# Optimization experiments

Hardware: AMD Instinct MI355X
Metric: run time of the kernel (lower is better)

The kernel has to match this reference:

```python
import jax, jax.numpy as jnp
import numpy as np

D = 512
SCALE = float(np.sqrt(D // 8))  # sqrt(d_k), d_k = d_model/num_heads = 64
EPS = 1e-5


def _ln(x, g, b):
    m = jnp.mean(x, axis=-1, keepdims=True)
    v = jnp.var(x, axis=-1, keepdims=True)
    return (x - m) * jax.lax.rsqrt(v + EPS) * g + b


def setup_inputs() -> dict:
    key = jax.random.key(0)
    ks = jax.random.split(key, 12)
    B, S = 512, 512
    w = lambda k, shp: jax.random.normal(k, shp, dtype=jnp.float32) * 0.02
    return {
        "sentiment_vec": jax.random.normal(ks[0], (B, D), dtype=jnp.float32),
        "price_sequence": jax.random.normal(ks[1], (B, S, D), dtype=jnp.float32),
        "Wq": w(ks[2], (D, D)), "bq": jnp.zeros((D,), jnp.float32),
        "Wk": w(ks[3], (D, D)), "bk": jnp.zeros((D,), jnp.float32),
        "Wv": w(ks[4], (D, D)), "bv": jnp.zeros((D,), jnp.float32),
        "Wo": w(ks[5], (D, D)), "bo": jnp.zeros((D,), jnp.float32),
        "Wg": w(ks[6], (2 * D, D)), "bg": jnp.zeros((D,), jnp.float32),
        "g_q": jnp.ones((D,), jnp.float32), "beta_q": jnp.zeros((D,), jnp.float32),
        "g_kv": jnp.ones((D,), jnp.float32), "beta_kv": jnp.zeros((D,), jnp.float32),
    }


def reference(sentiment_vec, price_sequence, Wq, bq, Wk, bk, Wv, bv, Wo, bo,
              Wg, bg, g_q, beta_q, g_kv, beta_kv):
    # LayerNorms (query is a single token per batch element)
    Q = _ln(sentiment_vec, g_q, beta_q)            # [B, D]
    KV = _ln(price_sequence, g_kv, beta_kv)        # [B, S, D]
    # Projections (note: forward never splits heads -> single-head attention)
    q = Q @ Wq + bq                                # [B, D]
    k = KV @ Wk + bk                               # [B, S, D]
    v = KV @ Wv + bv                               # [B, S, D]
    # Single-query attention
    scores = jnp.einsum('bd,bsd->bs', q, k) / SCALE
    attn = jax.nn.softmax(scores, axis=-1)         # [B, S] (dropout: eval mode)
    ctx = jnp.einsum('bs,bsd->bd', attn, v)        # [B, D]
    ctx = ctx @ Wo + bo
    # Sigmoid gate over concat([sentiment, context])
    gate_in = jnp.concatenate([sentiment_vec, ctx], axis=-1)  # [B, 2D]
    alpha = jax.nn.sigmoid(gate_in @ Wg + bg)
    fused = alpha * ctx + (1.0 - alpha) * sentiment_vec
    return fused, attn
```

## Files before the change

### kernel.cpp

```cpp
#include <hip/hip_runtime.h>

#define NB 512
#define NS 512
#define ND 512
#define INV_SCALE 0.125f
#define LN_EPS 1e-5f

typedef __attribute__((ext_vector_type(8))) short short8;
typedef __attribute__((ext_vector_type(4))) short short4v;
typedef __attribute__((ext_vector_type(4))) float float4v;

static __device__ __forceinline__ unsigned short f2bf(float x) {
    unsigned int u = __float_as_uint(x);
    unsigned int r = (u + 0x7fffu + ((u >> 16) & 1u)) >> 16;
    return (unsigned short)r;
}
static __device__ __forceinline__ float bf2f(unsigned short h) {
    return __uint_as_float(((unsigned int)h) << 16);
}

__global__ __launch_bounds__(64) void ln_rows_k(const float* __restrict__ x,
                                                const float* __restrict__ g,
                                                const float* __restrict__ be,
                                                float* __restrict__ y) {
    const int row = blockIdx.x;
    const int lane = threadIdx.x;
    const float* xr = x + (size_t)row * ND;
    float4 x0 = *(const float4*)(xr + 4 * lane);
    float4 x1 = *(const float4*)(xr + 256 + 4 * lane);
    float s1 = x0.x + x0.y + x0.z + x0.w + x1.x + x1.y + x1.z + x1.w;
    float s2 = x0.x * x0.x + x0.y * x0.y + x0.z * x0.z + x0.w * x0.w +
               x1.x * x1.x + x1.y * x1.y + x1.z * x1.z + x1.w * x1.w;
    for (int off = 32; off; off >>= 1) {
        s1 += __shfl_xor(s1, off, 64);
        s2 += __shfl_xor(s2, off, 64);
    }
    float mean = s1 * (1.f / 512.f);
    float rstd = rsqrtf(s2 * (1.f / 512.f) - mean * mean + LN_EPS);
    float4 g0 = *(const float4*)(g + 4 * lane);
    float4 g1 = *(const float4*)(g + 256 + 4 * lane);
    float4 b0 = *(const float4*)(be + 4 * lane);
    float4 b1 = *(const float4*)(be + 256 + 4 * lane);
    float4 y0, y1;
    y0.x = (x0.x - mean) * rstd * g0.x + b0.x;
    y0.y = (x0.y - mean) * rstd * g0.y + b0.y;
    y0.z = (x0.z - mean) * rstd * g0.z + b0.z;
    y0.w = (x0.w - mean) * rstd * g0.w + b0.w;
    y1.x = (x1.x - mean) * rstd * g1.x + b1.x;
    y1.y = (x1.y - mean) * rstd * g1.y + b1.y;
    y1.z = (x1.z - mean) * rstd * g1.z + b1.z;
    y1.w = (x1.w - mean) * rstd * g1.w + b1.w;
    float* yr = y + (size_t)row * ND;
    *(float4*)(yr + 4 * lane) = y0;
    *(float4*)(yr + 256 + 4 * lane) = y1;
}

__global__ __launch_bounds__(64) void rowdot_k(const float* __restrict__ q,
                                               const float* __restrict__ bk,
                                               float* __restrict__ s0) {
    const int row = blockIdx.x;
    const int lane = threadIdx.x;
    const float* qr = q + (size_t)row * ND;
    float4 a0 = *(const float4*)(qr + 4 * lane);
    float4 a1 = *(const float4*)(qr + 256 + 4 * lane);
    float4 c0 = *(const float4*)(bk + 4 * lane);
    float4 c1 = *(const float4*)(bk + 256 + 4 * lane);
    float d = a0.x * c0.x + a0.y * c0.y + a0.z * c0.z + a0.w * c0.w +
              a1.x * c1.x + a1.y * c1.y + a1.z * c1.z + a1.w * c1.w;
    for (int off = 32; off; off >>= 1) d += __shfl_xor(d, off, 64);
    if (lane == 0) s0[row] = d;
}

template <bool TRANS_B, int EPI>
__global__ __launch_bounds__(256) void gemm32_k(
    const float* __restrict__ A1, const float* __restrict__ A2, int ksplit,
    const float* __restrict__ B, const float* __restrict__ bias,
    float* __restrict__ C, int M, int N, int K,
    const float* __restrict__ e_ctx, const float* __restrict__ e_sent) {
    constexpr int LDK = 40;
    __shared__ __align__(16) unsigned short Ah[32 * LDK];
    __shared__ __align__(16) unsigned short Al[32 * LDK];
    __shared__ __align__(16) unsigned short Bh[32 * LDK];
    __shared__ __align__(16) unsigned short Bl[32 * LDK];
    const int t = threadIdx.x;
    const int wave = t >> 6, lane = t & 63;
    const int m0 = blockIdx.y * 32, n0 = blockIdx.x * 32;
    const int wm = (wave & 1) * 16, wn = (wave >> 1) * 16;

    float4v acc = (float4v){0.f, 0.f, 0.f, 0.f};

    const int arow = wm + (lane & 15);
    const int brow = wn + (lane & 15);
    const int kq8 = (lane >> 4) * 8;

    const int srow = t >> 3, skq = (t & 7) * 4;

    float4 va, vb;
    {
        int kg = skq;
        if (kg < ksplit)
            va = *(const float4*)(A1 + (size_t)(m0 + srow) * ksplit + kg);
        else
            va = *(const float4*)(A2 + (size_t)(m0 + srow) * (K - ksplit) + (kg - ksplit));
        if (TRANS_B)
            vb = *(const float4*)(B + (size_t)(n0 + srow) * K + skq);
        else
            vb = *(const float4*)(B + (size_t)srow * N + n0 + skq);
    }

    for (int k0 = 0; k0 < K; k0 += 32) {
        {
            unsigned short h0 = f2bf(va.x), h1 = f2bf(va.y), h2 = f2bf(va.z), h3 = f2bf(va.w);
            short4v hv = {(short)h0, (short)h1, (short)h2, (short)h3};
            short4v lv = {(short)f2bf(va.x - bf2f(h0)), (short)f2bf(va.y - bf2f(h1)),
                          (short)f2bf(va.z - bf2f(h2)), (short)f2bf(va.w - bf2f(h3))};
            *(short4v*)&Ah[srow * LDK + skq] = hv;
            *(short4v*)&Al[srow * LDK + skq] = lv;
        }
        if (TRANS_B) {
            unsigned short h0 = f2bf(vb.x), h1 = f2bf(vb.y), h2 = f2bf(vb.z), h3 = f2bf(vb.w);
            short4v hv = {(short)h0, (short)h1, (short)h2, (short)h3};
            short4v lv = {(short)f2bf(vb.x - bf2f(h0)), (short)f2bf(vb.y - bf2f(h1)),
                          (short)f2bf(vb.z - bf2f(h2)), (short)f2bf(vb.w - bf2f(h3))};
            *(short4v*)&Bh[srow * LDK + skq] = hv;
            *(short4v*)&Bl[srow * LDK + skq] = lv;
        } else {
            float vv[4] = {vb.x, vb.y, vb.z, vb.w};
#pragma unroll
            for (int j = 0; j < 4; ++j) {
                unsigned short hh = f2bf(vv[j]);
                Bh[(skq + j) * LDK + srow] = hh;
                Bl[(skq + j) * LDK + srow] = f2bf(vv[j] - bf2f(hh));
            }
        }
        float4 va2, vb2;
        if (k0 + 32 < K) {
            int kg = k0 + 32 + skq;
            if (kg < ksplit)
                va2 = *(const float4*)(A1 + (size_t)(m0 + srow) * ksplit + kg);
            else
                va2 = *(const float4*)(A2 + (size_t)(m0 + srow) * (K - ksplit) + (kg - ksplit));
            if (TRANS_B)
                vb2 = *(const float4*)(B + (size_t)(n0 + srow) * K + k0 + 32 + skq);
            else
                vb2 = *(const float4*)(B + (size_t)(k0 + 32 + srow) * N + n0 + skq);
        } else {
            va2 = va; vb2 = vb;
        }
        __syncthreads();
        short8 ah = *(const short8*)&Ah[arow * LDK + kq8];
        short8 al = *(const short8*)&Al[arow * LDK + kq8];
        short8 bh = *(const short8*)&Bh[brow * LDK + kq8];
        short8 bl = *(const short8*)&Bl[brow * LDK + kq8];
        acc = __builtin_amdgcn_mfma_f32_16x16x32_bf16(ah, bh, acc, 0, 0, 0);
        acc = __builtin_amdgcn_mfma_f32_16x16x32_bf16(ah, bl, acc, 0, 0, 0);
        acc = __builtin_amdgcn_mfma_f32_16x16x32_bf16(al, bh, acc, 0, 0, 0);
        __syncthreads();
        va = va2; vb = vb2;
    }

    const int coln = lane & 15, rbase = (lane >> 4) * 4;
    const int n = n0 + wn + coln;
    const float bv = bias ? bias[n] : 0.f;
#pragma unroll
    for (int r = 0; r < 4; ++r) {
        int m = m0 + wm + rbase + r;
        float val = acc[r] + bv;
        if (EPI == 1) {
            float a = 1.f / (1.f + __expf(-val));
            float cx = e_ctx[(size_t)m * N + n];
            float sv = e_sent[(size_t)m * N + n];
            val = a * cx + (1.f - a) * sv;
        }
        C[(size_t)m * N + n] = val;
    }
}

__global__ __launch_bounds__(512) void flash_k(const float* __restrict__ ps,
                                               const float* __restrict__ g,
                                               const float* __restrict__ be,
                                               const float* __restrict__ qp,
                                               const float* __restrict__ s0v,
                                               float* __restrict__ ctx_pre,
                                               float* __restrict__ attn) {
    const int b = blockIdx.x;
    const int t = threadIdx.x;
    const int wave = t >> 6, lane = t & 63;
    __shared__ float zbuf[NS];
    __shared__ float ubuf[8][ND];
    __shared__ float lw[8], tw[8];

    const float* qb = qp + (size_t)b * ND;
    float4 q0 = *(const float4*)(qb + 4 * lane);
    float4 q1 = *(const float4*)(qb + 256 + 4 * lane);
    float4 g0 = *(const float4*)(g + 4 * lane);
    float4 g1 = *(const float4*)(g + 256 + 4 * lane);
    float4 b0 = *(const float4*)(be + 4 * lane);
    float4 b1 = *(const float4*)(be + 256 + 4 * lane);

    float4 qg0, qg1;
    qg0.x = g0.x * q0.x; qg0.y = g0.y * q0.y; qg0.z = g0.z * q0.z; qg0.w = g0.w * q0.w;
    qg1.x = g1.x * q1.x; qg1.y = g1.y * q1.y; qg1.z = g1.z * q1.z; qg1.w = g1.w * q1.w;
    float c1 = qg0.x + qg0.y + qg0.z + qg0.w + qg1.x + qg1.y + qg1.z + qg1.w;
    float c2 = b0.x * q0.x + b0.y * q0.y + b0.z * q0.z + b0.w * q0.w +
               b1.x * q1.x + b1.y * q1.y + b1.z * q1.z + b1.w * q1.w;
    for (int off = 32; off; off >>= 1) {
        c1 += __shfl_xor(c1, off, 64);
        c2 += __shfl_xor(c2, off, 64);
    }
    const float K2 = INV_SCALE * (c2 + s0v[b]);
    const float C1 = c1;

    float l = 0.f, t1 = 0.f;
    float4 u0 = {0.f, 0.f, 0.f, 0.f}, u1 = {0.f, 0.f, 0.f, 0.f};

    const float* base = ps + ((size_t)b * NS + wave * 64) * ND + 4 * lane;
    float4 xa0 = *(const float4*)(base);
    float4 xa1 = *(const float4*)(base + 256);
    float4 xb0 = *(const float4*)(base + ND);
    float4 xb1 = *(const float4*)(base + ND + 256);

    for (int r = 0; r < 64; r += 2) {
        float4 ya0, ya1, yb0, yb1;
        if (r < 62) {
            const float* nb = base + (size_t)(r + 2) * ND;
            ya0 = *(const float4*)(nb);
            ya1 = *(const float4*)(nb + 256);
            yb0 = *(const float4*)(nb + ND);
            yb1 = *(const float4*)(nb + ND + 256);
        } else {
            ya0 = xa0; ya1 = xa1; yb0 = xb0; yb1 = xb1;
        }
        float sa1 = xa0.x + xa0.y + xa0.z + xa0.w + xa1.x + xa1.y + xa1.z + xa1.w;
        float sb1 = xb0.x + xb0.y + xb0.z + xb0.w + xb1.x + xb1.y + xb1.z + xb1.w;
        float sa2 = xa0.x * xa0.x + xa0.y * xa0.y + xa0.z * xa0.z + xa0.w * xa0.w +
                    xa1.x * xa1.x + xa1.y * xa1.y + xa1.z * xa1.z + xa1.w * xa1.w;
        float sb2 = xb0.x * xb0.x + xb0.y * xb0.y + xb0.z * xb0.z + xb0.w * xb0.w +
                    xb1.x * xb1.x + xb1.y * xb1.y + xb1.z * xb1.z + xb1.w * xb1.w;
        float sa3 = xa0.x * qg0.x + xa0.y * qg0.y + xa0.z * qg0.z + xa0.w * qg0.w +
                    xa1.x * qg1.x + xa1.y * qg1.y + xa1.z * qg1.z + xa1.w * qg1.w;
        float sb3 = xb0.x * qg0.x + xb0.y * qg0.y + xb0.z * qg0.z + xb0.w * qg0.w +
                    xb1.x * qg1.x + xb1.y * qg1.y + xb1.z * qg1.z + xb1.w * qg1.w;
        for (int off = 32; off; off >>= 1) {
            sa1 += __shfl_xor(sa1, off, 64);
            sb1 += __shfl_xor(sb1, off, 64);
            sa2 += __shfl_xor(sa2, off, 64);
            sb2 += __shfl_xor(sb2, off, 64);
            sa3 += __shfl_xor(sa3, off, 64);
            sb3 += __shfl_xor(sb3, off, 64);
        }
        float meana = sa1 * (1.f / 512.f), meanb = sb1 * (1.f / 512.f);
        float rstda = rsqrtf(sa2 * (1.f / 512.f) - meana * meana + LN_EPS);
        float rstdb = rsqrtf(sb2 * (1.f / 512.f) - meanb * meanb + LN_EPS);
        float za = INV_SCALE * rstda * (sa3 - meana * C1) + K2;
        float zb = INV_SCALE * rstdb * (sb3 - meanb * C1) + K2;
        float pa = __expf(za), pb = __expf(zb);
        l += pa + pb;
        float pra = pa * rstda, prb = pb * rstdb;
        t1 += pra * meana + prb * meanb;
        u0.x += pra * xa0.x + prb * xb0.x;
        u0.y += pra * xa0.y + prb * xb0.y;
        u0.z += pra * xa0.z + prb * xb0.z;
        u0.w += pra * xa0.w + prb * xb0.w;
        u1.x += pra * xa1.x + prb * xb1.x;
        u1.y += pra * xa1.y + prb * xb1.y;
        u1.z += pra * xa1.z + prb * xb1.z;
        u1.w += pra * xa1.w + prb * xb1.w;
        if (lane == 0) {
            zbuf[wave * 64 + r] = za;
            zbuf[wave * 64 + r + 1] = zb;
        }
        xa0 = ya0; xa1 = ya1; xb0 = yb0; xb1 = yb1;
    }

    *(float4*)&ubuf[wave][4 * lane] = u0;
    *(float4*)&ubuf[wave][256 + 4 * lane] = u1;
    if (lane == 0) { lw[wave] = l; tw[wave] = t1; }
    __syncthreads();

    float U = 0.f;
#pragma unroll
    for (int w = 0; w < 8; ++w) U += ubuf[w][t];
    float L = 0.f, T = 0.f;
#pragma unroll
    for (int w = 0; w < 8; ++w) { L += lw[w]; T += tw[w]; }
    float invL = 1.f / L;
    ctx_pre[(size_t)b * ND + t] = g[t] * (U - T) * invL + be[t];
    attn[(size_t)b * NS + t] = __expf(zbuf[t]) * invL;
}

extern "C" void kernel_launch(void* const* d_in, const int* in_sizes, int n_in,
                              void* d_out, int out_size, void* d_ws, size_t ws_size,
                              hipStream_t stream) {
    const float* sent = (const float*)d_in[0];
    const float* ps   = (const float*)d_in[1];
    const float* Wq = (const float*)d_in[2];
    const float* bq = (const float*)d_in[3];
    const float* Wk = (const float*)d_in[4];
    const float* bk = (const float*)d_in[5];
    const float* Wv = (const float*)d_in[6];
    const float* bv = (const float*)d_in[7];
    const float* Wo = (const float*)d_in[8];
    const float* bo = (const float*)d_in[9];
    const float* Wg = (const float*)d_in[10];
    const float* bg = (const float*)d_in[11];
    const float* g_q = (const float*)d_in[12];
    const float* beta_q = (const float*)d_in[13];
    const float* g_kv = (const float*)d_in[14];
    const float* beta_kv = (const float*)d_in[15];

    float* out = (float*)d_out;
    float* attn = out + NB * ND;

    float* ws = (float*)d_ws;
    float* Qln     = ws;
    float* q       = ws + 262144;
    float* qprime  = ws + 524288;
    float* s0      = ws + 786432;
    float* ctx_pre = ws + 786944;
    float* ctx1    = ws + 1049088;
    float* ctx2    = ws + 1311232;

    dim3 g32(16, 16);

    ln_rows_k<<<NB, 64, 0, stream>>>(sent, g_q, beta_q, Qln);
    gemm32_k<false, 0><<<g32, 256, 0, stream>>>(
        Qln, nullptr, 512, Wq, bq, q, 512, 512, 512, nullptr, nullptr);
    rowdot_k<<<NB, 64, 0, stream>>>(q, bk, s0);
    gemm32_k<true, 0><<<g32, 256, 0, stream>>>(
        q, nullptr, 512, Wk, nullptr, qprime, 512, 512, 512, nullptr, nullptr);

    flash_k<<<NB, 512, 0, stream>>>(ps, g_kv, beta_kv, qprime, s0, ctx_pre, attn);

    gemm32_k<false, 0><<<g32, 256, 0, stream>>>(
        ctx_pre, nullptr, 512, Wv, bv, ctx1, 512, 512, 512, nullptr, nullptr);
    gemm32_k<false, 0><<<g32, 256, 0, stream>>>(
        ctx1, nullptr, 512, Wo, bo, ctx2, 512, 512, 512, nullptr, nullptr);

    gemm32_k<false, 1><<<g32, 256, 0, stream>>>(
        sent, ctx2, 512, Wg, bg, out, 512, 512, 1024, ctx2, sent);
}
```

Baseline: 791.7 us.

## Precompose weight products and hide weight GEMMs inside the flash kernel

Folds Wq·Wkᵀ and Wv·Wo into combined weight matrices, and folds the bias terms into precomputed vectors, so the chain of activation GEMMs gets shorter (q→q' and ctx1→ctx2 each collapse to one GEMM). The Wv·Wo product and the sentiment half of the gate GEMM run as extra blocks appended to the flash kernel's grid, where they can overlap with the attention work. The gate GEMM now only processes the context half. This removes several launches and dependent GEMMs, at the cost of extra weight-only GEMMs per call and a larger union shared-memory footprint in the flash kernel.

```diff
diff --git a/kernel.cpp b/kernel.cpp
--- a/kernel.cpp
+++ b/kernel.cpp
@@ -19,10 +19,123 @@
     return __uint_as_float(((unsigned int)h) << 16);
 }
 
-__global__ __launch_bounds__(64) void ln_rows_k(const float* __restrict__ x,
-                                                const float* __restrict__ g,
-                                                const float* __restrict__ be,
-                                                float* __restrict__ y) {
+__global__ __launch_bounds__(256) void prep_k(
+    const float* __restrict__ Wq, const float* __restrict__ Wk,
+    const float* __restrict__ bq, const float* __restrict__ bk,
+    const float* __restrict__ bv, const float* __restrict__ Wo,
+    const float* __restrict__ bo,
+    float* __restrict__ Wqk, float* __restrict__ wv,
+    float* __restrict__ bqk, float* __restrict__ bvo, float* __restrict__ c0) {
+    const int bid = blockIdx.x;
+    const int t = threadIdx.x;
+    const int wave = t >> 6, lane = t & 63;
+
+    if (bid < 256) {
+        constexpr int LDK = 40;
+        __shared__ __align__(16) unsigned short Ah[32 * LDK];
+        __shared__ __align__(16) unsigned short Al[32 * LDK];
+        __shared__ __align__(16) unsigned short Bh[32 * LDK];
+        __shared__ __align__(16) unsigned short Bl[32 * LDK];
+        const int m0 = (bid >> 4) * 32, n0 = (bid & 15) * 32;
+        const int wm = (wave & 1) * 16, wn = (wave >> 1) * 16;
+        float4v acc = (float4v){0.f, 0.f, 0.f, 0.f};
+        const int arow = wm + (lane & 15);
+        const int brow = wn + (lane & 15);
+        const int kq8 = (lane >> 4) * 8;
+        const int srow = t >> 3, skq = (t & 7) * 4;
+
+        float4 va = *(const float4*)(Wq + (size_t)(m0 + srow) * 512 + skq);
+        float4 vb = *(const float4*)(Wk + (size_t)(n0 + srow) * 512 + skq);
+        for (int k0 = 0; k0 < 512; k0 += 32) {
+            {
+                unsigned short h0 = f2bf(va.x), h1 = f2bf(va.y), h2 = f2bf(va.z), h3 = f2bf(va.w);
+                short4v hv = {(short)h0, (short)h1, (short)h2, (short)h3};
+                short4v lv = {(short)f2bf(va.x - bf2f(h0)), (short)f2bf(va.y - bf2f(h1)),
+                              (short)f2bf(va.z - bf2f(h2)), (short)f2bf(va.w - bf2f(h3))};
+                *(short4v*)&Ah[srow * LDK + skq] = hv;
+                *(short4v*)&Al[srow * LDK + skq] = lv;
+            }
+            {
+                unsigned short h0 = f2bf(vb.x), h1 = f2bf(vb.y), h2 = f2bf(vb.z), h3 = f2bf(vb.w);
+                short4v hv = {(short)h0, (short)h1, (short)h2, (short)h3};
+                short4v lv = {(short)f2bf(vb.x - bf2f(h0)), (short)f2bf(vb.y - bf2f(h1)),
+                              (short)f2bf(vb.z - bf2f(h2)), (short)f2bf(vb.w - bf2f(h3))};
+                *(short4v*)&Bh[srow * LDK + skq] = hv;
+                *(short4v*)&Bl[srow * LDK + skq] = lv;
+            }
+            float4 va2, vb2;
+            if (k0 + 32 < 512) {
+                va2 = *(const float4*)(Wq + (size_t)(m0 + srow) * 512 + k0 + 32 + skq);
+                vb2 = *(const float4*)(Wk + (size_t)(n0 + srow) * 512 + k0 + 32 + skq);
+            } else { va2 = va; vb2 = vb; }
+            __syncthreads();
+            short8 ah = *(const short8*)&Ah[arow * LDK + kq8];
+            short8 al = *(const short8*)&Al[arow * LDK + kq8];
+            short8 bh = *(const short8*)&Bh[brow * LDK + kq8];
+            short8 bl = *(const short8*)&Bl[brow * LDK + kq8];
+            acc = __builtin_amdgcn_mfma_f32_16x16x32_bf16(ah, bh, acc, 0, 0, 0);
+            acc = __builtin_amdgcn_mfma_f32_16x16x32_bf16(ah, bl, acc, 0, 0, 0);
+            acc = __builtin_amdgcn_mfma_f32_16x16x32_bf16(al, bh, acc, 0, 0, 0);
+            __syncthreads();
+            va = va2; vb = vb2;
+        }
+        const int coln = lane & 15, rbase = (lane >> 4) * 4;
+        const int n = n0 + wn + coln;
+#pragma unroll
+        for (int r = 0; r < 4; ++r)
+            Wqk[(size_t)(m0 + wm + rbase + r) * 512 + n] = acc[r];
+    } else if (bid == 256) {
+        float4 k0v = *(const float4*)(bk + 4 * lane);
+        float4 k1v = *(const float4*)(bk + 256 + 4 * lane);
+        for (int m = wave; m < 512; m += 4) {
+            const float* r = Wq + (size_t)m * 512;
+            float4 a0 = *(const float4*)(r + 4 * lane);
+            float4 a1 = *(const float4*)(r + 256 + 4 * lane);
+            float d = a0.x * k0v.x + a0.y * k0v.y + a0.z * k0v.z + a0.w * k0v.w +
+                      a1.x * k1v.x + a1.y * k1v.y + a1.z * k1v.z + a1.w * k1v.w;
+            for (int off = 32; off; off >>= 1) d += __shfl_xor(d, off, 64);
+            if (lane == 0) wv[m] = d;
+        }
+    } else if (bid == 257) {
+        float4 q0v = *(const float4*)(bq + 4 * lane);
+        float4 q1v = *(const float4*)(bq + 256 + 4 * lane);
+        for (int n = wave; n < 512; n += 4) {
+            const float* r = Wk + (size_t)n * 512;
+            float4 a0 = *(const float4*)(r + 4 * lane);
+            float4 a1 = *(const float4*)(r + 256 + 4 * lane);
+            float d = a0.x * q0v.x + a0.y * q0v.y + a0.z * q0v.z + a0.w * q0v.w +
+                      a1.x * q1v.x + a1.y * q1v.y + a1.z * q1v.z + a1.w * q1v.w;
+            for (int off = 32; off; off >>= 1) d += __shfl_xor(d, off, 64);
+            if (lane == 0) bqk[n] = d;
+        }
+        if (wave == 0) {
+            float4 b0v = *(const float4*)(bk + 4 * lane);
+            float4 b1v = *(const float4*)(bk + 256 + 4 * lane);
+            float d = b0v.x * q0v.x + b0v.y * q0v.y + b0v.z * q0v.z + b0v.w * q0v.w +
+                      b1v.x * q1v.x + b1v.y * q1v.y + b1v.z * q1v.z + b1v.w * q1v.w;
+            for (int off = 32; off; off >>= 1) d += __shfl_xor(d, off, 64);
+            if (lane == 0) c0[0] = d;
+        }
+    } else {
+        float a0 = 0.f, a1 = 0.f;
+#pragma unroll 4
+        for (int k = 0; k < 512; ++k) {
+            float s = bv[k];
+            a0 = fmaf(s, Wo[(size_t)k * 512 + t], a0);
+            a1 = fmaf(s, Wo[(size_t)k * 512 + 256 + t], a1);
+        }
+        bvo[t] = a0 + bo[t];
+        bvo[t + 256] = a1 + bo[t + 256];
+    }
+}
+
+__global__ __launch_bounds__(64) void ln_s0_k(const float* __restrict__ x,
+                                              const float* __restrict__ g,
+                                              const float* __restrict__ be,
+                                              const float* __restrict__ wv,
+                                              const float* __restrict__ c0,
+                                              float* __restrict__ y,
+                                              float* __restrict__ s0) {
     const int row = blockIdx.x;
     const int lane = threadIdx.x;
     const float* xr = x + (size_t)row * ND;
@@ -53,30 +166,20 @@
     float* yr = y + (size_t)row * ND;
     *(float4*)(yr + 4 * lane) = y0;
     *(float4*)(yr + 256 + 4 * lane) = y1;
-}
-
-__global__ __launch_bounds__(64) void rowdot_k(const float* __restrict__ q,
-                                               const float* __restrict__ bk,
-                                               float* __restrict__ s0) {
-    const int row = blockIdx.x;
-    const int lane = threadIdx.x;
-    const float* qr = q + (size_t)row * ND;
-    float4 a0 = *(const float4*)(qr + 4 * lane);
-    float4 a1 = *(const float4*)(qr + 256 + 4 * lane);
-    float4 c0 = *(const float4*)(bk + 4 * lane);
-    float4 c1 = *(const float4*)(bk + 256 + 4 * lane);
-    float d = a0.x * c0.x + a0.y * c0.y + a0.z * c0.z + a0.w * c0.w +
-              a1.x * c1.x + a1.y * c1.y + a1.z * c1.z + a1.w * c1.w;
+    float4 w0 = *(const float4*)(wv + 4 * lane);
+    float4 w1 = *(const float4*)(wv + 256 + 4 * lane);
+    float d = y0.x * w0.x + y0.y * w0.y + y0.z * w0.z + y0.w * w0.w +
+              y1.x * w1.x + y1.y * w1.y + y1.z * w1.z + y1.w * w1.w;
     for (int off = 32; off; off >>= 1) d += __shfl_xor(d, off, 64);
-    if (lane == 0) s0[row] = d;
-}
-
-template <bool TRANS_B, int EPI>
+    if (lane == 0) s0[row] = d + c0[0];
+}
+
+template <int EPI>
 __global__ __launch_bounds__(256) void gemm32_k(
-    const float* __restrict__ A1, const float* __restrict__ A2, int ksplit,
-    const float* __restrict__ B, const float* __restrict__ bias,
-    float* __restrict__ C, int M, int N, int K,
-    const float* __restrict__ e_ctx, const float* __restrict__ e_sent) {
+    const float* __restrict__ A, const float* __restrict__ B,
+    const float* __restrict__ bias, float* __restrict__ C, int N, int K,
+    const float* __restrict__ e_ctx, const float* __restrict__ e_sent,
+    const float* __restrict__ e_add) {
     constexpr int LDK = 40;
     __shared__ __align__(16) unsigned short Ah[32 * LDK];
     __shared__ __align__(16) unsigned short Al[32 * LDK];
@@ -88,25 +191,13 @@
     const int wm = (wave & 1) * 16, wn = (wave >> 1) * 16;
 
     float4v acc = (float4v){0.f, 0.f, 0.f, 0.f};
-
     const int arow = wm + (lane & 15);
     const int brow = wn + (lane & 15);
     const int kq8 = (lane >> 4) * 8;
-
     const int srow = t >> 3, skq = (t & 7) * 4;
 
-    float4 va, vb;
-    {
-        int kg = skq;
-        if (kg < ksplit)
-            va = *(const float4*)(A1 + (size_t)(m0 + srow) * ksplit + kg);
-        else
-            va = *(const float4*)(A2 + (size_t)(m0 + srow) * (K - ksplit) + (kg - ksplit));
-        if (TRANS_B)
-            vb = *(const float4*)(B + (size_t)(n0 + srow) * K + skq);
-        else
-            vb = *(const float4*)(B + (size_t)srow * N + n0 + skq);
-    }
+    float4 va = *(const float4*)(A + (size_t)(m0 + srow) * K + skq);
+    float4 vb = *(const float4*)(B + (size_t)srow * N + n0 + skq);
 
     for (int k0 = 0; k0 < K; k0 += 32) {
         {
@@ -117,14 +208,7 @@
             *(short4v*)&Ah[srow * LDK + skq] = hv;
             *(short4v*)&Al[srow * LDK + skq] = lv;
         }
-        if (TRANS_B) {
-            unsigned short h0 = f2bf(vb.x), h1 = f2bf(vb.y), h2 = f2bf(vb.z), h3 = f2bf(vb.w);
-            short4v hv = {(short)h0, (short)h1, (short)h2, (short)h3};
-            short4v lv = {(short)f2bf(vb.x - bf2f(h0)), (short)f2bf(vb.y - bf2f(h1)),
-                          (short)f2bf(vb.z - bf2f(h2)), (short)f2bf(vb.w - bf2f(h3))};
-            *(short4v*)&Bh[srow * LDK + skq] = hv;
-            *(short4v*)&Bl[srow * LDK + skq] = lv;
-        } else {
+        {
             float vv[4] = {vb.x, vb.y, vb.z, vb.w};
 #pragma unroll
             for (int j = 0; j < 4; ++j) {
@@ -135,18 +219,9 @@
         }
         float4 va2, vb2;
         if (k0 + 32 < K) {
-            int kg = k0 + 32 + skq;
-            if (kg < ksplit)
-                va2 = *(const float4*)(A1 + (size_t)(m0 + srow) * ksplit + kg);
-            else
-                va2 = *(const float4*)(A2 + (size_t)(m0 + srow) * (K - ksplit) + (kg - ksplit));
-            if (TRANS_B)
-                vb2 = *(const float4*)(B + (size_t)(n0 + srow) * K + k0 + 32 + skq);
-            else
-                vb2 = *(const float4*)(B + (size_t)(k0 + 32 + srow) * N + n0 + skq);
-        } else {
-            va2 = va; vb2 = vb;
-        }
+            va2 = *(const float4*)(A + (size_t)(m0 + srow) * K + k0 + 32 + skq);
+            vb2 = *(const float4*)(B + (size_t)(k0 + 32 + srow) * N + n0 + skq);
+        } else { va2 = va; vb2 = vb; }
         __syncthreads();
         short8 ah = *(const short8*)&Ah[arow * LDK + kq8];
         short8 al = *(const short8*)&Al[arow * LDK + kq8];
@@ -161,13 +236,14 @@
 
     const int coln = lane & 15, rbase = (lane >> 4) * 4;
     const int n = n0 + wn + coln;
-    const float bv = bias ? bias[n] : 0.f;
+    const float bvv = bias ? bias[n] : 0.f;
 #pragma unroll
     for (int r = 0; r < 4; ++r) {
         int m = m0 + wm + rbase + r;
-        float val = acc[r] + bv;
-        if (EPI == 1) {
-            float a = 1.f / (1.f + __expf(-val));
+        float val = acc[r] + bvv;
+        if (EPI == 2) {
+            float z = val + e_add[(size_t)m * N + n];
+            float a = 1.f / (1.f + __expf(-z));
             float cx = e_ctx[(size_t)m * N + n];
             float sv = e_sent[(size_t)m * N + n];
             val = a * cx + (1.f - a) * sv;
@@ -176,117 +252,188 @@
     }
 }
 
-__global__ __launch_bounds__(512) void flash_k(const float* __restrict__ ps,
-                                               const float* __restrict__ g,
-                                               const float* __restrict__ be,
-                                               const float* __restrict__ qp,
-                                               const float* __restrict__ s0v,
-                                               float* __restrict__ ctx_pre,
-                                               float* __restrict__ attn) {
-    const int b = blockIdx.x;
+__global__ __launch_bounds__(512) void flash_fused_k(
+    const float* __restrict__ ps, const float* __restrict__ g,
+    const float* __restrict__ be, const float* __restrict__ qp,
+    const float* __restrict__ s0v, float* __restrict__ ctx_pre,
+    float* __restrict__ attn,
+    const float* __restrict__ Wv, const float* __restrict__ Wo,
+    float* __restrict__ Wvo,
+    const float* __restrict__ sent, const float* __restrict__ Wg,
+    const float* __restrict__ bg, float* __restrict__ sentg) {
+    union SMemU {
+        struct { float zbuf[NS]; float ubuf[8][ND]; float lw[8]; float tw[8]; } fl;
+        struct { unsigned short Ah[64 * 40]; unsigned short Al[64 * 40];
+                 unsigned short Bh[32 * 40]; unsigned short Bl[32 * 40]; } gm;
+    };
+    __shared__ __align__(16) SMemU sm;
+    const int bid = blockIdx.x;
     const int t = threadIdx.x;
     const int wave = t >> 6, lane = t & 63;
-    __shared__ float zbuf[NS];
-    __shared__ float ubuf[8][ND];
-    __shared__ float lw[8], tw[8];
-
-    const float* qb = qp + (size_t)b * ND;
-    float4 q0 = *(const float4*)(qb + 4 * lane);
-    float4 q1 = *(const float4*)(qb + 256 + 4 * lane);
-    float4 g0 = *(const float4*)(g + 4 * lane);
-    float4 g1 = *(const float4*)(g + 256 + 4 * lane);
-    float4 b0 = *(const float4*)(be + 4 * lane);
-    float4 b1 = *(const float4*)(be + 256 + 4 * lane);
-
-    float4 qg0, qg1;
-    qg0.x = g0.x * q0.x; qg0.y = g0.y * q0.y; qg0.z = g0.z * q0.z; qg0.w = g0.w * q0.w;
-    qg1.x = g1.x * q1.x; qg1.y = g1.y * q1.y; qg1.z = g1.z * q1.z; qg1.w = g1.w * q1.w;
-    float c1 = qg0.x + qg0.y + qg0.z + qg0.w + qg1.x + qg1.y + qg1.z + qg1.w;
-    float c2 = b0.x * q0.x + b0.y * q0.y + b0.z * q0.z + b0.w * q0.w +
-               b1.x * q1.x + b1.y * q1.y + b1.z * q1.z + b1.w * q1.w;
-    for (int off = 32; off; off >>= 1) {
-        c1 += __shfl_xor(c1, off, 64);
-        c2 += __shfl_xor(c2, off, 64);
+
+    if (bid < 512) {
+        const int b = bid;
+        const float* qb = qp + (size_t)b * ND;
+        float4 q0 = *(const float4*)(qb + 4 * lane);
+        float4 q1 = *(const float4*)(qb + 256 + 4 * lane);
+        float4 g0 = *(const float4*)(g + 4 * lane);
+        float4 g1 = *(const float4*)(g + 256 + 4 * lane);
+        float4 b0 = *(const float4*)(be + 4 * lane);
+        float4 b1 = *(const float4*)(be + 256 + 4 * lane);
+
+        float4 qg0, qg1;
+        qg0.x = g0.x * q0.x; qg0.y = g0.y * q0.y; qg0.z = g0.z * q0.z; qg0.w = g0.w * q0.w;
+        qg1.x = g1.x * q1.x; qg1.y = g1.y * q1.y; qg1.z = g1.z * q1.z; qg1.w = g1.w * q1.w;
+        float c1 = qg0.x + qg0.y + qg0.z + qg0.w + qg1.x + qg1.y + qg1.z + qg1.w;
+        float c2 = b0.x * q0.x + b0.y * q0.y + b0.z * q0.z + b0.w * q0.w +
+                   b1.x * q1.x + b1.y * q1.y + b1.z * q1.z + b1.w * q1.w;
+        for (int off = 32; off; off >>= 1) {
+            c1 += __shfl_xor(c1, off, 64);
+            c2 += __shfl_xor(c2, off, 64);
+        }
+        const float K2 = INV_SCALE * (c2 + s0v[b]);
+        const float C1 = c1;
+
+        float l = 0.f, t1 = 0.f;
+        float4 u0 = {0.f, 0.f, 0.f, 0.f}, u1 = {0.f, 0.f, 0.f, 0.f};
+
+        const float* base = ps + ((size_t)b * NS + wave * 64) * ND + 4 * lane;
+        float4 xa0 = *(const float4*)(base);
+        float4 xa1 = *(const float4*)(base + 256);
+        float4 xb0 = *(const float4*)(base + ND);
+        float4 xb1 = *(const float4*)(base + ND + 256);
+
+        for (int r = 0; r < 64; r += 2) {
+            float4 ya0, ya1, yb0, yb1;
+            if (r < 62) {
+                const float* nb = base + (size_t)(r + 2) * ND;
+                ya0 = *(const float4*)(nb);
+                ya1 = *(const float4*)(nb + 256);
+                yb0 = *(const float4*)(nb + ND);
+                yb1 = *(const float4*)(nb + ND + 256);
+            } else {
+                ya0 = xa0; ya1 = xa1; yb0 = xb0; yb1 = xb1;
+            }
+            float sa1 = xa0.x + xa0.y + xa0.z + xa0.w + xa1.x + xa1.y + xa1.z + xa1.w;
+            float sb1 = xb0.x + xb0.y + xb0.z + xb0.w + xb1.x + xb1.y + xb1.z + xb1.w;
+            float sa2 = xa0.x * xa0.x + xa0.y * xa0.y + xa0.z * xa0.z + xa0.w * xa0.w +
+                        xa1.x * xa1.x + xa1.y * xa1.y + xa1.z * xa1.z + xa1.w * xa1.w;
+            float sb2 = xb0.x * xb0.x + xb0.y * xb0.y + xb0.z * xb0.z + xb0.w * xb0.w +
+                        xb1.x * xb1.x + xb1.y * xb1.y + xb1.z * xb1.z + xb1.w * xb1.w;
+            float sa3 = xa0.x * qg0.x + xa0.y * qg0.y + xa0.z * qg0.z + xa0.w * qg0.w +
+                        xa1.x * qg1.x + xa1.y * qg1.y + xa1.z * qg1.z + xa1.w * qg1.w;
+            float sb3 = xb0.x * qg0.x + xb0.y * qg0.y + xb0.z * qg0.z + xb0.w * qg0.w +
+                        xb1.x * qg1.x + xb1.y * qg1.y + xb1.z * qg1.z + xb1.w * qg1.w;
+            for (int off = 32; off; off >>= 1) {
+                sa1 += __shfl_xor(sa1, off, 64);
+                sb1 += __shfl_xor(sb1, off, 64);
+                sa2 += __shfl_xor(sa2, off, 64);
+                sb2 += __shfl_xor(sb2, off, 64);
+                sa3 += __shfl_xor(sa3, off, 64);
+                sb3 += __shfl_xor(sb3, off, 64);
+            }
+            float meana = sa1 * (1.f / 512.f), meanb = sb1 * (1.f / 512.f);
+            float rstda = rsqrtf(sa2 * (1.f / 512.f) - meana * meana + LN_EPS);
+            float rstdb = rsqrtf(sb2 * (1.f / 512.f) - meanb * meanb + LN_EPS);
+            float za = INV_SCALE * rstda * (sa3 - meana * C1) + K2;
+            float zb = INV_SCALE * rstdb * (sb3 - meanb * C1) + K2;
+            float pa = __expf(za), pb = __expf(zb);
+            l += pa + pb;
+            float pra = pa * rstda, prb = pb * rstdb;
+            t1 += pra * meana + prb * meanb;
+            u0.x += pra * xa0.x + prb * xb0.x;
+            u0.y += pra * xa0.y + prb * xb0.y;
+            u0.z += pra * xa0.z + prb * xb0.z;
+            u0.w += pra * xa0.w + prb * xb0.w;
+            u1.x += pra * xa1.x + prb * xb1.x;
+            u1.y += pra * xa1.y + prb * xb1.y;
+            u1.z += pra * xa1.z + prb * xb1.z;
+            u1.w += pra * xa1.w + prb * xb1.w;
+            if (lane == 0) {
+                sm.fl.zbuf[wave * 64 + r] = za;
+                sm.fl.zbuf[wave * 64 + r + 1] = zb;
+            }
+            xa0 = ya0; xa1 = ya1; xb0 = yb0; xb1 = yb1;
+        }
+
+        *(float4*)&sm.fl.ubuf[wave][4 * lane] = u0;
+        *(float4*)&sm.fl.ubuf[wave][256 + 4 * lane] = u1;
+        if (lane == 0) { sm.fl.lw[wave] = l; sm.fl.tw[wave] = t1; }
+        __syncthreads();
+
+        float U = 0.f;
+#pragma unroll
+        for (int w = 0; w < 8; ++w) U += sm.fl.ubuf[w][t];
+        float L = 0.f, T = 0.f;
+#pragma unroll
+        for (int w = 0; w < 8; ++w) { L += sm.fl.lw[w]; T += sm.fl.tw[w]; }
+        float invL = 1.f / L;
+        ctx_pre[(size_t)b * ND + t] = g[t] * (U - T) * invL + be[t];
+        attn[(size_t)b * NS + t] = __expf(sm.fl.zbuf[t]) * invL;
+    } else {
+        constexpr int LDK = 40;
+        int gb = bid - 512;
+        const float* A; const float* B; const float* bias; float* C;
+        if (gb < 128) { A = Wv; B = Wo; bias = nullptr; C = Wvo; }
+        else { gb -= 128; A = sent; B = Wg; bias = bg; C = sentg; }
+        const int m0 = (gb >> 4) * 64, n0 = (gb & 15) * 32;
+        const int wm = (wave & 3) * 16, wn = (wave >> 2) * 16;
+        float4v acc = (float4v){0.f, 0.f, 0.f, 0.f};
+        const int arow = wm + (lane & 15);
+        const int brow = wn + (lane & 15);
+        const int kq8 = (lane >> 4) * 8;
+        const int srow = t >> 3, skq = (t & 7) * 4;
+        unsigned short* Ah = sm.gm.Ah;
+        unsigned short* Al = sm.gm.Al;
+        unsigned short* Bh = sm.gm.Bh;
+        unsigned short* Bl = sm.gm.Bl;
+
+        float4 va = *(const float4*)(A + (size_t)(m0 + srow) * 512 + skq);
+        float4 vb = {0.f, 0.f, 0.f, 0.f};
+        const int bkrow = t >> 3, bnq = (t & 7) * 4;
+        if (t < 256) vb = *(const float4*)(B + (size_t)bkrow * 512 + n0 + bnq);
+
+        for (int k0 = 0; k0 < 512; k0 += 32) {
+            {
+                unsigned short h0 = f2bf(va.x), h1 = f2bf(va.y), h2 = f2bf(va.z), h3 = f2bf(va.w);
+                short4v hv = {(short)h0, (short)h1, (short)h2, (short)h3};
+                short4v lv = {(short)f2bf(va.x - bf2f(h0)), (short)f2bf(va.y - bf2f(h1)),
+                              (short)f2bf(va.z - bf2f(h2)), (short)f2bf(va.w - bf2f(h3))};
+                *(short4v*)&Ah[srow * LDK + skq] = hv;
+                *(short4v*)&Al[srow * LDK + skq] = lv;
+            }
+            if (t < 256) {
+                float vv[4] = {vb.x, vb.y, vb.z, vb.w};
+#pragma unroll
+                for (int j = 0; j < 4; ++j) {
+                    unsigned short hh = f2bf(vv[j]);
+                    Bh[(bnq + j) * LDK + bkrow] = hh;
+                    Bl[(bnq + j) * LDK + bkrow] = f2bf(vv[j] - bf2f(hh));
+                }
+            }
+            float4 va2 = va, vb2 = vb;
+            if (k0 + 32 < 512) {
+                va2 = *(const float4*)(A + (size_t)(m0 + srow) * 512 + k0 + 32 + skq);
+                if (t < 256) vb2 = *(const float4*)(B + (size_t)(k0 + 32 + bkrow) * 512 + n0 + bnq);
+            }
+            __syncthreads();
+            short8 ah = *(const short8*)&Ah[arow * LDK + kq8];
+            short8 al = *(const short8*)&Al[arow * LDK + kq8];
+            short8 bh = *(const short8*)&Bh[brow * LDK + kq8];
+            short8 bl = *(const short8*)&Bl[brow * LDK + kq8];
+            acc = __builtin_amdgcn_mfma_f32_16x16x32_bf16(ah, bh, acc, 0, 0, 0);
+            acc = __builtin_amdgcn_mfma_f32_16x16x32_bf16(ah, bl, acc, 0, 0, 0);
+            acc = __builtin_amdgcn_mfma_f32_16x16x32_bf16(al, bh, acc, 0, 0, 0);
+            __syncthreads();
+            va = va2; vb = vb2;
+        }
+        const int coln = lane & 15, rbase = (lane >> 4) * 4;
+        const int n = n0 + wn + coln;
+        const float bvv = bias ? bias[n] : 0.f;
+#pragma unroll
+        for (int r = 0; r < 4; ++r)
+            C[(size_t)(m0 + wm + rbase + r) * 512 + n] = acc[r] + bvv;
     }
-    const float K2 = INV_SCALE * (c2 + s0v[b]);
-    const float C1 = c1;
-
-    float l = 0.f, t1 = 0.f;
-    float4 u0 = {0.f, 0.f, 0.f, 0.f}, u1 = {0.f, 0.f, 0.f, 0.f};
-
-    const float* base = ps + ((size_t)b * NS + wave * 64) * ND + 4 * lane;
-    float4 xa0 = *(const float4*)(base);
-    float4 xa1 = *(const float4*)(base + 256);
-    float4 xb0 = *(const float4*)(base + ND);
-    float4 xb1 = *(const float4*)(base + ND + 256);
-
-    for (int r = 0; r < 64; r += 2) {
-        float4 ya0, ya1, yb0, yb1;
-        if (r < 62) {
-            const float* nb = base + (size_t)(r + 2) * ND;
-            ya0 = *(const float4*)(nb);
-            ya1 = *(const float4*)(nb + 256);
-            yb0 = *(const float4*)(nb + ND);
-            yb1 = *(const float4*)(nb + ND + 256);
-        } else {
-            ya0 = xa0; ya1 = xa1; yb0 = xb0; yb1 = xb1;
-        }
-        float sa1 = xa0.x + xa0.y + xa0.z + xa0.w + xa1.x + xa1.y + xa1.z + xa1.w;
-        float sb1 = xb0.x + xb0.y + xb0.z + xb0.w + xb1.x + xb1.y + xb1.z + xb1.w;
-        float sa2 = xa0.x * xa0.x + xa0.y * xa0.y + xa0.z * xa0.z + xa0.w * xa0.w +
-                    xa1.x * xa1.x + xa1.y * xa1.y + xa1.z * xa1.z + xa1.w * xa1.w;
-        float sb2 = xb0.x * xb0.x + xb0.y * xb0.y + xb0.z * xb0.z + xb0.w * xb0.w +
-                    xb1.x * xb1.x + xb1.y * xb1.y + xb1.z * xb1.z + xb1.w * xb1.w;
-        float sa3 = xa0.x * qg0.x + xa0.y * qg0.y + xa0.z * qg0.z + xa0.w * qg0.w +
-                    xa1.x * qg1.x + xa1.y * qg1.y + xa1.z * qg1.z + xa1.w * qg1.w;
-        float sb3 = xb0.x * qg0.x + xb0.y * qg0.y + xb0.z * qg0.z + xb0.w * qg0.w +
-                    xb1.x * qg1.x + xb1.y * qg1.y + xb1.z * qg1.z + xb1.w * qg1.w;
-        for (int off = 32; off; off >>= 1) {
-            sa1 += __shfl_xor(sa1, off, 64);
-            sb1 += __shfl_xor(sb1, off, 64);
-            sa2 += __shfl_xor(sa2, off, 64);
-            sb2 += __shfl_xor(sb2, off, 64);
-            sa3 += __shfl_xor(sa3, off, 64);
-            sb3 += __shfl_xor(sb3, off, 64);
-        }
-        float meana = sa1 * (1.f / 512.f), meanb = sb1 * (1.f / 512.f);
-        float rstda = rsqrtf(sa2 * (1.f / 512.f) - meana * meana + LN_EPS);
-        float rstdb = rsqrtf(sb2 * (1.f / 512.f) - meanb * meanb + LN_EPS);
-        float za = INV_SCALE * rstda * (sa3 - meana * C1) + K2;
-        float zb = INV_SCALE * rstdb * (sb3 - meanb * C1) + K2;
-        float pa = __expf(za), pb = __expf(zb);
-        l += pa + pb;
-        float pra = pa * rstda, prb = pb * rstdb;
-        t1 += pra * meana + prb * meanb;
-        u0.x += pra * xa0.x + prb * xb0.x;
-        u0.y += pra * xa0.y + prb * xb0.y;
-        u0.z += pra * xa0.z + prb * xb0.z;
-        u0.w += pra * xa0.w + prb * xb0.w;
-        u1.x += pra * xa1.x + prb * xb1.x;
-        u1.y += pra * xa1.y + prb * xb1.y;
-        u1.z += pra * xa1.z + prb * xb1.z;
-        u1.w += pra * xa1.w + prb * xb1.w;
-        if (lane == 0) {
-            zbuf[wave * 64 + r] = za;
-            zbuf[wave * 64 + r + 1] = zb;
-        }
-        xa0 = ya0; xa1 = ya1; xb0 = yb0; xb1 = yb1;
-    }
-
-    *(float4*)&ubuf[wave][4 * lane] = u0;
-    *(float4*)&ubuf[wave][256 + 4 * lane] = u1;
-    if (lane == 0) { lw[wave] = l; tw[wave] = t1; }
-    __syncthreads();
-
-    float U = 0.f;
-#pragma unroll
-    for (int w = 0; w < 8; ++w) U += ubuf[w][t];
-    float L = 0.f, T = 0.f;
-#pragma unroll
-    for (int w = 0; w < 8; ++w) { L += lw[w]; T += tw[w]; }
-    float invL = 1.f / L;
-    ctx_pre[(size_t)b * ND + t] = g[t] * (U - T) * invL + be[t];
-    attn[(size_t)b * NS + t] = __expf(zbuf[t]) * invL;
 }
 
 extern "C" void kernel_launch(void* const* d_in, const int* in_sizes, int n_in,
@@ -313,30 +460,31 @@
     float* attn = out + NB * ND;
 
     float* ws = (float*)d_ws;
-    float* Qln     = ws;
-    float* q       = ws + 262144;
+    float* Wqk     = ws;
+    float* Qln     = ws + 262144;
     float* qprime  = ws + 524288;
-    float* s0      = ws + 786432;
-    float* ctx_pre = ws + 786944;
-    float* ctx1    = ws + 1049088;
-    float* ctx2    = ws + 1311232;
+    float* ctx_pre = ws + 786432;
+    float* Wvo     = ws + 1048576;
+    float* sentg   = ws + 1310720;
+    float* ctx2    = ws + 1572864;
+    float* wv      = ws + 1835008;
+    float* bqk     = ws + 1835520;
+    float* bvo     = ws + 1836032;
+    float* s0      = ws + 1836544;
+    float* c0      = ws + 1837056;
 
     dim3 g32(16, 16);
 
-    ln_rows_k<<<NB, 64, 0, stream>>>(sent, g_q, beta_q, Qln);
-    gemm32_k<false, 0><<<g32, 256, 0, stream>>>(
-        Qln, nullptr, 512, Wq, bq, q, 512, 512, 512, nullptr, nullptr);
-    rowdot_k<<<NB, 64, 0, stream>>>(q, bk, s0);
-    gemm32_k<true, 0><<<g32, 256, 0, stream>>>(
-        q, nullptr, 512, Wk, nullptr, qprime, 512, 512, 512, nullptr, nullptr);
-
-    flash_k<<<NB, 512, 0, stream>>>(ps, g_kv, beta_kv, qprime, s0, ctx_pre, attn);
-
-    gemm32_k<false, 0><<<g32, 256, 0, stream>>>(
-        ctx_pre, nullptr, 512, Wv, bv, ctx1, 512, 512, 512, nullptr, nullptr);
-    gemm32_k<false, 0><<<g32, 256, 0, stream>>>(
-        ctx1, nullptr, 512, Wo, bo, ctx2, 512, 512, 512, nullptr, nullptr);
-
-    gemm32_k<false, 1><<<g32, 256, 0, stream>>>(
-        sent, ctx2, 512, Wg, bg, out, 512, 512, 1024, ctx2, sent);
-}
+    prep_k<<<259, 256, 0, stream>>>(Wq, Wk, bq, bk, bv, Wo, bo,
+                                    Wqk, wv, bqk, bvo, c0);
+    ln_s0_k<<<NB, 64, 0, stream>>>(sent, g_q, beta_q, wv, c0, Qln, s0);
+    gemm32_k<0><<<g32, 256, 0, stream>>>(Qln, Wqk, bqk, qprime, 512, 512,
+                                         nullptr, nullptr, nullptr);
+    flash_fused_k<<<768, 512, 0, stream>>>(ps, g_kv, beta_kv, qprime, s0,
+                                           ctx_pre, attn, Wv, Wo, Wvo,
+                                           sent, Wg, bg, sentg);
+    gemm32_k<0><<<g32, 256, 0, stream>>>(ctx_pre, Wvo, bvo, ctx2, 512, 512,
+                                         nullptr, nullptr, nullptr);
+    gemm32_k<2><<<g32, 256, 0, stream>>>(ctx2, Wg + 512 * 512, nullptr, out,
+                                         512, 512, ctx2, sent, sentg);
+}
```

Result: slower. 817.2 us (+3.2%).
